# Performance work log

Hardware: AMD Instinct MI355X
Metric: run time of the kernel (lower is better)

The kernel has to match this reference:

```python
import jax, jax.numpy as jnp
import numpy as np
import math

H = 1024
N = 64          # d_state; complex modes = N // 2
N2 = N // 2
B = 8
L = 2048
DT_MIN, DT_MAX = 0.001, 0.1


def setup_inputs() -> dict:
    key = jax.random.key(0)
    ks = jax.random.split(key, 8)
    u = jax.random.normal(ks[0], (B, H, L), dtype=jnp.float32)
    # log_dt ~ Uniform[log(dt_min), log(dt_max)]
    log_dt = (jax.random.uniform(ks[1], (H,), dtype=jnp.float32)
              * (math.log(DT_MAX) - math.log(DT_MIN)) + math.log(DT_MIN))
    # random_dplr with scaling='inverse': real part 0.5, imag = (1/pi)*N*(N/(1+2n)-1)
    n = jnp.arange(N2, dtype=jnp.float32)
    w_real = 0.5 * jnp.ones((1, N2), dtype=jnp.float32)
    w_imag = ((1.0 / math.pi) * N * (N / (1.0 + 2.0 * n) - 1.0))[None, :].astype(jnp.float32)
    log_w_real = jnp.log(w_real + 1e-4)  # module stores log(-w.real + 1e-4)
    # C = randn complex (channels=1, H, N2), scaled by normalized B (folded into randn here)
    C_re = jax.random.normal(ks[2], (1, H, N2), dtype=jnp.float32) / math.sqrt(2 * N2)
    C_im = jax.random.normal(ks[3], (1, H, N2), dtype=jnp.float32) / math.sqrt(2 * N2)
    D = jax.random.normal(ks[4], (1, H), dtype=jnp.float32)
    # output_linear: Conv1d(k=1) from channels*H -> H  => weight (H, H)
    W_out = jax.random.normal(ks[5], (H, H), dtype=jnp.float32) / math.sqrt(H)
    b_out = jax.random.normal(ks[6], (H,), dtype=jnp.float32) * 0.01
    return {"u": u, "log_dt": log_dt, "log_w_real": log_w_real, "w_imag": w_imag,
            "C_re": C_re, "C_im": C_im, "D": D, "W_out": W_out, "b_out": b_out}


def reference(u, log_dt, log_w_real, w_imag, C_re, C_im, D, W_out, b_out):
    b, h, l = u.shape
    # --- SSKernelDiag.forward ---
    dt = jnp.exp(log_dt)                                   # (H,)
    w = -jnp.exp(log_w_real) + 1j * w_imag                 # (n_ssm=1, N2)
    w = jnp.broadcast_to(w, (h, w.shape[-1]))              # repeat copies -> (H, N2)
    dtA = w * dt[:, None]                                  # (H, N2) complex
    C = (C_re + 1j * C_im) * (jnp.exp(dtA) - 1.0) / w      # (c, H, N2)
    # Vandermonde: exp(dtA * arange(L)) -> (H, N2, L) complex
    K = jnp.exp(dtA[:, :, None] * jnp.arange(l, dtype=jnp.float32))
    k = 2.0 * jnp.einsum('chn,hnl->chl', C, K).real        # (c, H, L) float
    # --- FFT convolution ---
    k_f = jnp.fft.rfft(k, n=2 * l)                         # (c, H, L+1)
    u_f = jnp.fft.rfft(u, n=2 * l)                         # (B, H, L+1)
    y_f = jnp.einsum('bhl,chl->bchl', u_f, k_f)
    y = jnp.fft.irfft(y_f, n=2 * l)[..., :l]               # (B, c, H, L)
    # skip connection with D
    y = y + jnp.einsum('bhl,ch->bchl', u, D)
    y = y.reshape(b, -1, l)                                # (B, c*H, L)
    y = jax.nn.gelu(y, approximate=False)
    # output 1x1 conv: (B, c*H, L) x (H, c*H) -> (B, H, L)
    y = jnp.einsum('bil,oi->bol', y, W_out) + b_out[None, :, None]
    return y
```

## Files before the change

kernel.cpp:

```cpp
#include <hip/hip_runtime.h>
#include <hip/hip_bf16.h>

#define HH 1024
#define LL 2048
#define BB 8
#define NN2 32
#define CT 128
#define NCH 16

typedef short bf16x8 __attribute__((ext_vector_type(8)));
typedef float f32x4  __attribute__((ext_vector_type(4)));

static __device__ __forceinline__ unsigned short bfbits(float x) {
    __hip_bfloat16 h = __float2bfloat16(x);
    return *(unsigned short*)&h;
}
static __device__ __forceinline__ float f_from_bits(unsigned short b) {
    __hip_bfloat16 h; *(unsigned short*)&h = b; return __bfloat162float(h);
}
static __device__ __forceinline__ float2 cexp_n(float2 dA, float p) {
    float mag = __expf(dA.x * p);
    float rev = dA.y * p * 0.15915494309f;
    rev -= floorf(rev);
    float ang = rev * 6.28318530718f;
    return make_float2(mag * __cosf(ang), mag * __sinf(ang));
}

#define SWZ(off, row) ((off) ^ (((row) & 7) << 4))

__global__ __launch_bounds__(256) void aux_tables(
    const float* __restrict__ log_dt, const float* __restrict__ log_w_real,
    const float* __restrict__ w_imag, const float* __restrict__ C_re,
    const float* __restrict__ C_im,
    __hip_bfloat16* __restrict__ AJ_g, __hip_bfloat16* __restrict__ AP_g,
    float* __restrict__ misc_g)
{
    __shared__ float2 dtA_s[NN2];
    __shared__ float2 Cn_s[NN2];
    const int tid = threadIdx.x;
    const int h = blockIdx.x;

    if (tid < NN2) {
        int n = tid;
        float dt = expf(log_dt[h]);
        float wr = -expf(log_w_real[n]);
        float wi = w_imag[n];
        float dar = wr * dt, dai = wi * dt;
        dtA_s[n] = make_float2(dar, dai);
        float er = expf(dar);
        float sn, cs; sincosf(dai, &sn, &cs);
        float exr = er * cs - 1.0f, exi = er * sn;
        float den = wr * wr + wi * wi;
        float fr = (exr * wr + exi * wi) / den;
        float fi = (exi * wr - exr * wi) / den;
        float cre = C_re[h * NN2 + n], cim = C_im[h * NN2 + n];
        float2 Cv = make_float2(cre * fr - cim * fi, cre * fi + cim * fr);
        Cn_s[n] = Cv;
        misc_g[h * 256 + 128 + 2 * n]     = Cv.x;
        misc_g[h * 256 + 128 + 2 * n + 1] = Cv.y;
        float magA = expf(dar * 128.0f);
        float snA, csA; sincosf(dai * 128.0f, &snA, &csA);
        misc_g[h * 256 + 192 + 2 * n]     = magA * csA;
        misc_g[h * 256 + 192 + 2 * n + 1] = magA * snA;
    }
    __syncthreads();

    char* ajb = (char*)AJ_g + (size_t)h * 16384;
    #pragma unroll
    for (int q = 0; q < 2; ++q) {
        int task = q * 256 + tid;
        int n = task >> 4, j0 = (task & 15) * 8;
        float2 dA = dtA_s[n];
        unsigned rw[4], iw[4];
        #pragma unroll
        for (int i2 = 0; i2 < 4; ++i2) {
            float2 a0 = cexp_n(dA, (float)(127 - j0 - 2 * i2));
            float2 a1 = cexp_n(dA, (float)(127 - j0 - 2 * i2 - 1));
            rw[i2] = (unsigned)bfbits(a0.x) | ((unsigned)bfbits(a1.x) << 16);
            iw[i2] = (unsigned)bfbits(a0.y) | ((unsigned)bfbits(a1.y) << 16);
        }
        int r0 = 2 * n, r1 = 2 * n + 1;
        *(uint4*)(ajb + SWZ(r0 * 256 + j0 * 2, r0)) = make_uint4(rw[0], rw[1], rw[2], rw[3]);
        *(uint4*)(ajb + SWZ(r1 * 256 + j0 * 2, r1)) = make_uint4(iw[0], iw[1], iw[2], iw[3]);
    }

    char* apb = (char*)AP_g + (size_t)h * 16384;
    #pragma unroll
    for (int q = 0; q < 2; ++q) {
        int task = q * 256 + tid;
        int ttr = task >> 2, n0 = (task & 3) * 8;
        unsigned w[8];
        #pragma unroll
        for (int i = 0; i < 8; ++i) {
            float2 a = cexp_n(dtA_s[n0 + i], (float)(ttr + 1));
            w[i] = (unsigned)bfbits(2.0f * a.x) | ((unsigned)bfbits(-2.0f * a.y) << 16);
        }
        *(uint4*)(apb + SWZ(ttr * 128 + n0 * 4, ttr))      = make_uint4(w[0], w[1], w[2], w[3]);
        *(uint4*)(apb + SWZ(ttr * 128 + n0 * 4 + 16, ttr)) = make_uint4(w[4], w[5], w[6], w[7]);
    }

    {
        int t = tid >> 1, nb = (tid & 1) * 16;
        float s = 0.f;
        #pragma unroll
        for (int i = 0; i < 16; ++i) {
            int n = nb + i;
            float2 a = cexp_n(dtA_s[n], (float)t);
            float2 C = Cn_s[n];
            s += C.x * a.x - C.y * a.y;
        }
        s += __shfl_xor(s, 1);
        if ((tid & 1) == 0) misc_g[h * 256 + t] = 2.0f * s;
    }
}

#define S_U    0
#define S_UN   16384
#define S_P    32768
#define S_KT   40960
#define S_TOT  41984

#define KBUILD(hf)                                                       \
    _Pragma("unroll")                                                    \
    for (int q = 0; q < 4; ++q) {                                        \
        int idx = q * 512 + tid;                                         \
        int ttr = idx >> 4, j0 = (idx & 15) * 4;                         \
        int base = ttr - (hf) * 64 - j0;                                 \
        ushort4 o;                                                       \
        o.x = (base     >= 0) ? bfbits(kt[base])     : (unsigned short)0;\
        o.y = (base - 1 >= 0) ? bfbits(kt[base - 1]) : (unsigned short)0;\
        o.z = (base - 2 >= 0) ? bfbits(kt[base - 2]) : (unsigned short)0;\
        o.w = (base - 3 >= 0) ? bfbits(kt[base - 3]) : (unsigned short)0;\
        *(ushort4*)(smem + SWZ(S_UN + ttr * 128 + j0 * 2, ttr)) = o;     \
    }

__global__ __launch_bounds__(512, 6) void ssm_mfma(
    const float* __restrict__ u,
    const __hip_bfloat16* __restrict__ AJ_g,
    const __hip_bfloat16* __restrict__ AP_g,
    const float* __restrict__ misc_g,
    const float* __restrict__ Dp, __hip_bfloat16* __restrict__ g_out)
{
    extern __shared__ char smem[];
    float*  kt   = (float*)(smem + S_KT);
    float2* CnL  = (float2*)(smem + S_KT + 512);
    float2* A128 = (float2*)(smem + S_KT + 768);

    const int tid  = threadIdx.x;
    const int lane = tid & 63;
    const int wave = tid >> 6;
    const int wm   = wave >> 2;
    const int wn   = wave & 3;
    const int h    = blockIdx.x;
    const int bh   = blockIdx.y;

    {
        const char* ajs = (const char*)AJ_g + (size_t)h * 16384;
        __builtin_amdgcn_global_load_lds(
            (const __attribute__((address_space(1))) void*)(ajs + tid * 16),
            (__attribute__((address_space(3))) void*)(smem + S_UN + wave * 1024), 16, 0, 0);
        __builtin_amdgcn_global_load_lds(
            (const __attribute__((address_space(1))) void*)(ajs + 8192 + tid * 16),
            (__attribute__((address_space(3))) void*)(smem + S_UN + 8192 + wave * 1024), 16, 0, 0);
        if (tid < 64) {
            const char* ms = (const char*)misc_g + (size_t)h * 1024;
            __builtin_amdgcn_global_load_lds(
                (const __attribute__((address_space(1))) void*)(ms + tid * 16),
                (__attribute__((address_space(3))) void*)(smem + S_KT), 16, 0, 0);
        }
    }

    float4 ureg[4];
    #pragma unroll
    for (int q = 0; q < 4; ++q) {
        int b = bh * 4 + q;
        ureg[q] = *(const float4*)(u + ((size_t)(b * HH + h)) * LL + tid * 4);
    }
    #pragma unroll
    for (int q = 0; q < 4; ++q) {
        int row = q * 16 + (tid >> 5);
        int j   = (tid & 31) * 4;
        ushort4 o;
        o.x = bfbits(ureg[q].x); o.y = bfbits(ureg[q].y);
        o.z = bfbits(ureg[q].z); o.w = bfbits(ureg[q].w);
        *(ushort4*)(smem + SWZ(S_U + row * 256 + j * 2, row)) = o;
    }
    asm volatile("s_waitcnt vmcnt(0)" ::: "memory");
    __syncthreads();

    f32x4 accP[2] = {};
    #pragma unroll
    for (int ks = 0; ks < 4; ++ks) {
        int kf = ks * 32 + (lane >> 4) * 8;
        bf16x8 a0, a1, b0;
        {
            int r = wm * 32 + (lane & 15);
            a0 = *(bf16x8*)(smem + SWZ(S_U + r * 256 + kf * 2, r));
            int r2 = r + 16;
            a1 = *(bf16x8*)(smem + SWZ(S_U + r2 * 256 + kf * 2, r2));
        }
        {
            int r = wn * 16 + (lane & 15);
            b0 = *(bf16x8*)(smem + SWZ(S_UN + r * 256 + kf * 2, r));
        }
        accP[0] = __builtin_amdgcn_mfma_f32_16x16x32_bf16(a0, b0, accP[0], 0, 0, 0);
        accP[1] = __builtin_amdgcn_mfma_f32_16x16x32_bf16(a1, b0, accP[1], 0, 0, 0);
    }
    #pragma unroll
    for (int mt = 0; mt < 2; ++mt)
        #pragma unroll
        for (int r = 0; r < 4; ++r) {
            int row = wm * 32 + mt * 16 + (lane >> 4) * 4 + r;
            int col = wn * 16 + (lane & 15);
            *(unsigned short*)(smem + SWZ(S_P + row * 128 + col * 2, row)) =
                bfbits(accP[mt][r]);
        }
    __syncthreads();

    KBUILD(0)
    if (tid < 128) {
        int b = tid >> 5, n = tid & 31;
        float2 C = CnL[n];
        float2 A = A128[n];
        float sr = 0.f, si = 0.f;
        for (int c = 0; c < NCH; ++c) {
            int row = b * 16 + c;
            int off = SWZ(S_P + row * 128 + n * 4, row);
            unsigned int pv = *(unsigned int*)(smem + off);
            float pr = f_from_bits((unsigned short)(pv & 0xffff));
            float pi = f_from_bits((unsigned short)(pv >> 16));
            float csr = C.x * sr - C.y * si;
            float csi = C.x * si + C.y * sr;
            *(unsigned int*)(smem + off) =
                (unsigned)bfbits(csr) | ((unsigned)bfbits(csi) << 16);
            float nsr = A.x * sr - A.y * si + pr;
            float nsi = A.x * si + A.y * sr + pi;
            sr = nsr; si = nsi;
        }
    }
    __syncthreads();

    f32x4 acc[2][2] = {};
    #pragma unroll
    for (int ks = 0; ks < 2; ++ks) {
        int kf = ks * 32 + (lane >> 4) * 8;
        bf16x8 a0, a1, bv[2];
        {
            int r = wm * 32 + (lane & 15);
            a0 = *(bf16x8*)(smem + SWZ(S_U + r * 256 + kf * 2, r));
            int r2 = r + 16;
            a1 = *(bf16x8*)(smem + SWZ(S_U + r2 * 256 + kf * 2, r2));
        }
        #pragma unroll
        for (int nt = 0; nt < 2; ++nt) {
            int ttr = wn * 32 + nt * 16 + (lane & 15);
            bv[nt] = *(bf16x8*)(smem + SWZ(S_UN + ttr * 128 + kf * 2, ttr));
        }
        #pragma unroll
        for (int nt = 0; nt < 2; ++nt) {
            acc[0][nt] = __builtin_amdgcn_mfma_f32_16x16x32_bf16(a0, bv[nt], acc[0][nt], 0, 0, 0);
            acc[1][nt] = __builtin_amdgcn_mfma_f32_16x16x32_bf16(a1, bv[nt], acc[1][nt], 0, 0, 0);
        }
    }
    __syncthreads();

    KBUILD(1)
    __syncthreads();
    #pragma unroll
    for (int ks = 0; ks < 2; ++ks) {
        int kf = ks * 32 + (lane >> 4) * 8;
        bf16x8 a0, a1, bv[2];
        {
            int r = wm * 32 + (lane & 15);
            a0 = *(bf16x8*)(smem + SWZ(S_U + r * 256 + 128 + kf * 2, r));
            int r2 = r + 16;
            a1 = *(bf16x8*)(smem + SWZ(S_U + r2 * 256 + 128 + kf * 2, r2));
        }
        #pragma unroll
        for (int nt = 0; nt < 2; ++nt) {
            int ttr = wn * 32 + nt * 16 + (lane & 15);
            bv[nt] = *(bf16x8*)(smem + SWZ(S_UN + ttr * 128 + kf * 2, ttr));
        }
        #pragma unroll
        for (int nt = 0; nt < 2; ++nt) {
            acc[0][nt] = __builtin_amdgcn_mfma_f32_16x16x32_bf16(a0, bv[nt], acc[0][nt], 0, 0, 0);
            acc[1][nt] = __builtin_amdgcn_mfma_f32_16x16x32_bf16(a1, bv[nt], acc[1][nt], 0, 0, 0);
        }
    }
    __syncthreads();

    {
        const char* aps = (const char*)AP_g + (size_t)h * 16384;
        __builtin_amdgcn_global_load_lds(
            (const __attribute__((address_space(1))) void*)(aps + tid * 16),
            (__attribute__((address_space(3))) void*)(smem + S_UN + wave * 1024), 16, 0, 0);
        __builtin_amdgcn_global_load_lds(
            (const __attribute__((address_space(1))) void*)(aps + 8192 + tid * 16),
            (__attribute__((address_space(3))) void*)(smem + S_UN + 8192 + wave * 1024), 16, 0, 0);
    }
    asm volatile("s_waitcnt vmcnt(0)" ::: "memory");
    __syncthreads();

    #pragma unroll
    for (int ks = 0; ks < 2; ++ks) {
        int kf = ks * 32 + (lane >> 4) * 8;
        bf16x8 a0, a1, bv[2];
        {
            int r = wm * 32 + (lane & 15);
            a0 = *(bf16x8*)(smem + SWZ(S_P + r * 128 + kf * 2, r));
            int r2 = r + 16;
            a1 = *(bf16x8*)(smem + SWZ(S_P + r2 * 128 + kf * 2, r2));
        }
        #pragma unroll
        for (int nt = 0; nt < 2; ++nt) {
            int ttr = wn * 32 + nt * 16 + (lane & 15);
            bv[nt] = *(bf16x8*)(smem + SWZ(S_UN + ttr * 128 + kf * 2, ttr));
        }
        #pragma unroll
        for (int nt = 0; nt < 2; ++nt) {
            acc[0][nt] = __builtin_amdgcn_mfma_f32_16x16x32_bf16(a0, bv[nt], acc[0][nt], 0, 0, 0);
            acc[1][nt] = __builtin_amdgcn_mfma_f32_16x16x32_bf16(a1, bv[nt], acc[1][nt], 0, 0, 0);
        }
    }

    const float Dv = Dp[h];
    #pragma unroll
    for (int mt = 0; mt < 2; ++mt)
        #pragma unroll
        for (int nt = 0; nt < 2; ++nt)
            #pragma unroll
            for (int r = 0; r < 4; ++r) {
                int row = wm * 32 + mt * 16 + (lane >> 4) * 4 + r;
                int ttr = wn * 32 + nt * 16 + (lane & 15);
                int off = SWZ(S_U + row * 256 + ttr * 2, row);
                float uv = f_from_bits(*(unsigned short*)(smem + off));
                float y = acc[mt][nt][r] + Dv * uv;
                float z = 0.7978845608f * (y + 0.044715f * y * y * y);
                float e = __expf(2.0f * z);
                float th = 1.0f - 2.0f / (e + 1.0f);
                float gel = 0.5f * y * (1.0f + th);
                *(unsigned short*)(smem + off) = bfbits(gel);
            }
    __syncthreads();
    #pragma unroll
    for (int q = 0; q < 2; ++q) {
        int flat = q * 512 + tid;
        int row = flat >> 4, c16 = flat & 15;
        uint4 v = *(uint4*)(smem + SWZ(S_U + row * 256 + c16 * 16, row));
        int b = bh * 4 + (row >> 4), c = row & 15;
        *(uint4*)(g_out + ((size_t)(b * HH + h)) * LL + c * CT + c16 * 8) = v;
    }
}

__global__ __launch_bounds__(256) void conv_w(
    const float* __restrict__ W, __hip_bfloat16* __restrict__ Wb)
{
    int i = blockIdx.x * 256 + threadIdx.x;
    float4 v = ((const float4*)W)[i];
    ushort4 o;
    o.x = bfbits(v.x); o.y = bfbits(v.y); o.z = bfbits(v.z); o.w = bfbits(v.w);
    ((ushort4*)Wb)[i] = o;
}

__global__ __launch_bounds__(256) void transpose_g(
    const __hip_bfloat16* __restrict__ g, __hip_bfloat16* __restrict__ gT)
{
    __shared__ __hip_bfloat16 t[64][66];
    const int tid = threadIdx.x;
    const int b  = blockIdx.z;
    const int h0 = blockIdx.x * 64;
    const int l0 = blockIdx.y * 64;

    #pragma unroll
    for (int q = 0; q < 2; ++q) {
        int idx = tid + q * 256;
        int r = idx >> 3, c8 = (idx & 7) * 8;
        uint4 v = *(const uint4*)(g + ((size_t)(b * HH + h0 + r)) * LL + l0 + c8);
        unsigned int* dst = (unsigned int*)&t[r][c8];
        dst[0] = v.x; dst[1] = v.y; dst[2] = v.z; dst[3] = v.w;
    }
    __syncthreads();
    #pragma unroll
    for (int q = 0; q < 2; ++q) {
        int idx = tid + q * 256;
        int r = idx >> 3, c8 = (idx & 7) * 8;
        unsigned short tmp[8];
        #pragma unroll
        for (int j = 0; j < 8; ++j) tmp[j] = *(unsigned short*)&t[c8 + j][r];
        uint4 o;
        o.x = (unsigned)tmp[0] | ((unsigned)tmp[1] << 16);
        o.y = (unsigned)tmp[2] | ((unsigned)tmp[3] << 16);
        o.z = (unsigned)tmp[4] | ((unsigned)tmp[5] << 16);
        o.w = (unsigned)tmp[6] | ((unsigned)tmp[7] << 16);
        *(uint4*)(gT + ((size_t)(b * LL + l0 + r)) * HH + h0 + c8) = o;
    }
}

#define GSLOT 32768
#define STAGE_TILE(kt_, s_)                                                      \
    {                                                                            \
        const int k0_ = (kt_) * 64;                                              \
        _Pragma("unroll")                                                        \
        for (int v_ = 0; v_ < 4; ++v_) {                                         \
            int row_ = v_ * 64 + rsub;                                           \
            const __hip_bfloat16* ga_ = Wb + (size_t)(o0 + row_) * HH + k0_ + csw; \
            const __hip_bfloat16* gb_ = gT + (size_t)(n0 + row_) * HH + k0_ + csw; \
            char* dA_ = smem + (s_) * GSLOT + (v_ * 64 + wave * 8) * 128;        \
            char* dB_ = smem + 2 * GSLOT + (s_) * GSLOT + (v_ * 64 + wave * 8) * 128; \
            __builtin_amdgcn_global_load_lds(                                    \
                (const __attribute__((address_space(1))) void*)ga_,              \
                (__attribute__((address_space(3))) void*)dA_, 16, 0, 0);         \
            __builtin_amdgcn_global_load_lds(                                    \
                (const __attribute__((address_space(1))) void*)gb_,              \
                (__attribute__((address_space(3))) void*)dB_, 16, 0, 0);         \
        }                                                                        \
    }

#define COMPUTE_TILE(s_)                                                         \
    {                                                                            \
        const char* baseA = smem + (s_) * GSLOT;                                 \
        const char* baseB = smem + 2 * GSLOT + (s_) * GSLOT;                     \
        bf16x8 bfr[4][2];                                                        \
        _Pragma("unroll")                                                        \
        for (int nt = 0; nt < 4; ++nt)                                           \
            _Pragma("unroll")                                                    \
            for (int ks = 0; ks < 2; ++ks) {                                     \
                int rb = wn * 64 + nt * 16 + (lane & 15);                        \
                int c  = (ks * 32 + (lane >> 4) * 8) ^ ((rb & 7) << 3);          \
                bfr[nt][ks] = *(const bf16x8*)(baseB + rb * 128 + c * 2);        \
            }                                                                    \
        _Pragma("unroll")                                                        \
        for (int qq = 0; qq < 4; ++qq) {                                         \
            bf16x8 af[2][2];                                                     \
            _Pragma("unroll")                                                    \
            for (int mt = 0; mt < 2; ++mt)                                       \
                _Pragma("unroll")                                                \
                for (int ks = 0; ks < 2; ++ks) {                                 \
                    int ra = wm * 128 + (qq * 2 + mt) * 16 + (lane & 15);        \
                    int c  = (ks * 32 + (lane >> 4) * 8) ^ ((ra & 7) << 3);      \
                    af[mt][ks] = *(const bf16x8*)(baseA + ra * 128 + c * 2);     \
                }                                                                \
            __builtin_amdgcn_s_setprio(1);                                       \
            _Pragma("unroll")                                                    \
            for (int mt = 0; mt < 2; ++mt)                                       \
                _Pragma("unroll")                                                \
                for (int nt = 0; nt < 4; ++nt) {                                 \
                    acc[qq * 2 + mt][nt] = __builtin_amdgcn_mfma_f32_16x16x32_bf16( \
                        af[mt][0], bfr[nt][0], acc[qq * 2 + mt][nt], 0, 0, 0);   \
                    acc[qq * 2 + mt][nt] = __builtin_amdgcn_mfma_f32_16x16x32_bf16( \
                        af[mt][1], bfr[nt][1], acc[qq * 2 + mt][nt], 0, 0, 0);   \
                }                                                                \
            __builtin_amdgcn_s_setprio(0);                                       \
        }                                                                        \
    }

__global__ __launch_bounds__(512, 2) void out_gemm_256(
    const __hip_bfloat16* __restrict__ Wb,
    const __hip_bfloat16* __restrict__ gT,
    const float* __restrict__ bias,
    float* __restrict__ out)
{
    extern __shared__ char smem[];
    const int tid  = threadIdx.x;
    const int lane = tid & 63;
    const int wave = tid >> 6;
    const int wm = wave >> 2;
    const int wn = wave & 3;

    int wg  = blockIdx.x;
    int swz = (wg & 7) * 32 + (wg >> 3);
    const int o0 = (swz & 3) * 256;
    const int n0 = (swz >> 2) * 256;

    const int rsub = tid >> 3;
    const int csw  = ((tid & 7) ^ (rsub & 7)) << 3;

    f32x4 acc[8][4] = {};

    STAGE_TILE(0, 0)
    STAGE_TILE(1, 1)

    for (int t = 0; t < 15; ++t) {
        asm volatile("s_waitcnt vmcnt(8)" ::: "memory");
        __builtin_amdgcn_s_barrier();
        __builtin_amdgcn_sched_barrier(0);
        COMPUTE_TILE(t & 1)
        asm volatile("s_waitcnt lgkmcnt(0)" ::: "memory");
        __builtin_amdgcn_s_barrier();
        __builtin_amdgcn_sched_barrier(0);
        if (t < 14) STAGE_TILE(t + 2, t & 1)
    }
    asm volatile("s_waitcnt vmcnt(0)" ::: "memory");
    __builtin_amdgcn_s_barrier();
    __builtin_amdgcn_sched_barrier(0);
    COMPUTE_TILE(1)

    const int bb = n0 >> 11;
    #pragma unroll
    for (int m = 0; m < 8; ++m) {
        int o = o0 + wm * 128 + m * 16 + (lane >> 4) * 4;
        #pragma unroll
        for (int nt = 0; nt < 4; ++nt) {
            int n = n0 + wn * 64 + nt * 16 + (lane & 15);
            int l = n & 2047;
            #pragma unroll
            for (int r = 0; r < 4; ++r)
                out[((size_t)(bb * HH + o + r)) * LL + l] = acc[m][nt][r] + bias[o + r];
        }
    }
}

extern "C" void kernel_launch(void* const* d_in, const int* in_sizes, int n_in,
                              void* d_out, int out_size, void* d_ws, size_t ws_size,
                              hipStream_t stream) {
    const float* u          = (const float*)d_in[0];
    const float* log_dt     = (const float*)d_in[1];
    const float* log_w_real = (const float*)d_in[2];
    const float* w_imag     = (const float*)d_in[3];
    const float* C_re       = (const float*)d_in[4];
    const float* C_im       = (const float*)d_in[5];
    const float* Dp         = (const float*)d_in[6];
    const float* W          = (const float*)d_in[7];
    const float* bias       = (const float*)d_in[8];
    float* out = (float*)d_out;

    __hip_bfloat16* AJ_g = (__hip_bfloat16*)d_out;
    __hip_bfloat16* AP_g = (__hip_bfloat16*)((char*)d_out + 16777216);
    __hip_bfloat16* g    = (__hip_bfloat16*)((char*)d_out + 33554432);
    __hip_bfloat16* gT     = (__hip_bfloat16*)d_ws;
    __hip_bfloat16* Wb     = (__hip_bfloat16*)((char*)d_ws + 33554432);
    float*          misc_g = (float*)((char*)d_ws + 35651584);

    hipFuncSetAttribute((const void*)ssm_mfma,
                        hipFuncAttributeMaxDynamicSharedMemorySize, S_TOT);
    hipFuncSetAttribute((const void*)out_gemm_256,
                        hipFuncAttributeMaxDynamicSharedMemorySize, 131072);

    conv_w<<<dim3(HH * HH / 1024), 256, 0, stream>>>(W, Wb);
    aux_tables<<<dim3(HH), 256, 0, stream>>>(log_dt, log_w_real, w_imag,
                                             C_re, C_im, AJ_g, AP_g, misc_g);
    ssm_mfma<<<dim3(HH, 2), 512, S_TOT, stream>>>(u, AJ_g, AP_g, misc_g, Dp, g);
    transpose_g<<<dim3(HH / 64, LL / 64, BB), 256, 0, stream>>>(g, gT);
    out_gemm_256<<<dim3(256), 512, 131072, stream>>>(Wb, gT, bias, out);
}
```

Baseline: 108.4 us.

## Process all eight batches per block in SSM kernel to reuse per-channel tables

The SSM chunked-scan kernel now handles all 8 batch rows for a channel in one block instead of splitting batches across two blocks. Each wave computes a larger 32x64 output tile, so the per-channel AJ/AP tables and kernel Toeplitz builds are loaded and built once per channel rather than twice. In exchange, shared memory per block grows and occupancy hints drop from 6 to 4 blocks, and the grid halves to 1024 blocks, which lowers parallelism.

```diff
diff --git a/kernel.cpp b/kernel.cpp
--- a/kernel.cpp
+++ b/kernel.cpp
@@ -115,10 +115,10 @@
 }
 
 #define S_U    0
-#define S_UN   16384
-#define S_P    32768
-#define S_KT   40960
-#define S_TOT  41984
+#define S_UN   32768
+#define S_P    49152
+#define S_KT   65536
+#define S_TOT  66560
 
 #define KBUILD(hf)                                                       \
     _Pragma("unroll")                                                    \
@@ -134,7 +134,7 @@
         *(ushort4*)(smem + SWZ(S_UN + ttr * 128 + j0 * 2, ttr)) = o;     \
     }
 
-__global__ __launch_bounds__(512, 6) void ssm_mfma(
+__global__ __launch_bounds__(512, 4) void ssm_mfma(
     const float* __restrict__ u,
     const __hip_bfloat16* __restrict__ AJ_g,
     const __hip_bfloat16* __restrict__ AP_g,
@@ -149,10 +149,9 @@
     const int tid  = threadIdx.x;
     const int lane = tid & 63;
     const int wave = tid >> 6;
-    const int wm   = wave >> 2;
-    const int wn   = wave & 3;
+    const int wr4  = wave >> 1;
+    const int wc2  = wave & 1;
     const int h    = blockIdx.x;
-    const int bh   = blockIdx.y;
 
     {
         const char* ajs = (const char*)AJ_g + (size_t)h * 16384;
@@ -170,14 +169,12 @@
         }
     }
 
-    float4 ureg[4];
-    #pragma unroll
-    for (int q = 0; q < 4; ++q) {
-        int b = bh * 4 + q;
-        ureg[q] = *(const float4*)(u + ((size_t)(b * HH + h)) * LL + tid * 4);
-    }
-    #pragma unroll
-    for (int q = 0; q < 4; ++q) {
+    float4 ureg[8];
+    #pragma unroll
+    for (int q = 0; q < 8; ++q)
+        ureg[q] = *(const float4*)(u + ((size_t)(q * HH + h)) * LL + tid * 4);
+    #pragma unroll
+    for (int q = 0; q < 8; ++q) {
         int row = q * 16 + (tid >> 5);
         int j   = (tid & 31) * 4;
         ushort4 o;
@@ -188,37 +185,43 @@
     asm volatile("s_waitcnt vmcnt(0)" ::: "memory");
     __syncthreads();
 
-    f32x4 accP[2] = {};
+    f32x4 accP[2][2] = {};
     #pragma unroll
     for (int ks = 0; ks < 4; ++ks) {
         int kf = ks * 32 + (lane >> 4) * 8;
-        bf16x8 a0, a1, b0;
+        bf16x8 a0, a1, b0, b1;
         {
-            int r = wm * 32 + (lane & 15);
+            int r = wr4 * 32 + (lane & 15);
             a0 = *(bf16x8*)(smem + SWZ(S_U + r * 256 + kf * 2, r));
             int r2 = r + 16;
             a1 = *(bf16x8*)(smem + SWZ(S_U + r2 * 256 + kf * 2, r2));
         }
         {
-            int r = wn * 16 + (lane & 15);
+            int r = wc2 * 32 + (lane & 15);
             b0 = *(bf16x8*)(smem + SWZ(S_UN + r * 256 + kf * 2, r));
-        }
-        accP[0] = __builtin_amdgcn_mfma_f32_16x16x32_bf16(a0, b0, accP[0], 0, 0, 0);
-        accP[1] = __builtin_amdgcn_mfma_f32_16x16x32_bf16(a1, b0, accP[1], 0, 0, 0);
+            int r2 = r + 16;
+            b1 = *(bf16x8*)(smem + SWZ(S_UN + r2 * 256 + kf * 2, r2));
+        }
+        accP[0][0] = __builtin_amdgcn_mfma_f32_16x16x32_bf16(a0, b0, accP[0][0], 0, 0, 0);
+        accP[0][1] = __builtin_amdgcn_mfma_f32_16x16x32_bf16(a0, b1, accP[0][1], 0, 0, 0);
+        accP[1][0] = __builtin_amdgcn_mfma_f32_16x16x32_bf16(a1, b0, accP[1][0], 0, 0, 0);
+        accP[1][1] = __builtin_amdgcn_mfma_f32_16x16x32_bf16(a1, b1, accP[1][1], 0, 0, 0);
     }
     #pragma unroll
     for (int mt = 0; mt < 2; ++mt)
         #pragma unroll
-        for (int r = 0; r < 4; ++r) {
-            int row = wm * 32 + mt * 16 + (lane >> 4) * 4 + r;
-            int col = wn * 16 + (lane & 15);
-            *(unsigned short*)(smem + SWZ(S_P + row * 128 + col * 2, row)) =
-                bfbits(accP[mt][r]);
-        }
+        for (int nt = 0; nt < 2; ++nt)
+            #pragma unroll
+            for (int r = 0; r < 4; ++r) {
+                int row = wr4 * 32 + mt * 16 + (lane >> 4) * 4 + r;
+                int col = wc2 * 32 + nt * 16 + (lane & 15);
+                *(unsigned short*)(smem + SWZ(S_P + row * 128 + col * 2, row)) =
+                    bfbits(accP[mt][nt][r]);
+            }
     __syncthreads();
 
     KBUILD(0)
-    if (tid < 128) {
+    if (tid < 256) {
         int b = tid >> 5, n = tid & 31;
         float2 C = CnL[n];
         float2 A = A128[n];
@@ -240,24 +243,24 @@
     }
     __syncthreads();
 
-    f32x4 acc[2][2] = {};
+    f32x4 acc[2][4] = {};
     #pragma unroll
     for (int ks = 0; ks < 2; ++ks) {
         int kf = ks * 32 + (lane >> 4) * 8;
-        bf16x8 a0, a1, bv[2];
+        bf16x8 a0, a1, bv[4];
         {
-            int r = wm * 32 + (lane & 15);
+            int r = wr4 * 32 + (lane & 15);
             a0 = *(bf16x8*)(smem + SWZ(S_U + r * 256 + kf * 2, r));
             int r2 = r + 16;
             a1 = *(bf16x8*)(smem + SWZ(S_U + r2 * 256 + kf * 2, r2));
         }
         #pragma unroll
-        for (int nt = 0; nt < 2; ++nt) {
-            int ttr = wn * 32 + nt * 16 + (lane & 15);
+        for (int nt = 0; nt < 4; ++nt) {
+            int ttr = wc2 * 64 + nt * 16 + (lane & 15);
             bv[nt] = *(bf16x8*)(smem + SWZ(S_UN + ttr * 128 + kf * 2, ttr));
         }
         #pragma unroll
-        for (int nt = 0; nt < 2; ++nt) {
+        for (int nt = 0; nt < 4; ++nt) {
             acc[0][nt] = __builtin_amdgcn_mfma_f32_16x16x32_bf16(a0, bv[nt], acc[0][nt], 0, 0, 0);
             acc[1][nt] = __builtin_amdgcn_mfma_f32_16x16x32_bf16(a1, bv[nt], acc[1][nt], 0, 0, 0);
         }
@@ -269,20 +272,20 @@
     #pragma unroll
     for (int ks = 0; ks < 2; ++ks) {
         int kf = ks * 32 + (lane >> 4) * 8;
-        bf16x8 a0, a1, bv[2];
+        bf16x8 a0, a1, bv[4];
         {
-            int r = wm * 32 + (lane & 15);
+            int r = wr4 * 32 + (lane & 15);
             a0 = *(bf16x8*)(smem + SWZ(S_U + r * 256 + 128 + kf * 2, r));
             int r2 = r + 16;
             a1 = *(bf16x8*)(smem + SWZ(S_U + r2 * 256 + 128 + kf * 2, r2));
         }
         #pragma unroll
-        for (int nt = 0; nt < 2; ++nt) {
-            int ttr = wn * 32 + nt * 16 + (lane & 15);
+        for (int nt = 0; nt < 4; ++nt) {
+            int ttr = wc2 * 64 + nt * 16 + (lane & 15);
             bv[nt] = *(bf16x8*)(smem + SWZ(S_UN + ttr * 128 + kf * 2, ttr));
         }
         #pragma unroll
-        for (int nt = 0; nt < 2; ++nt) {
+        for (int nt = 0; nt < 4; ++nt) {
             acc[0][nt] = __builtin_amdgcn_mfma_f32_16x16x32_bf16(a0, bv[nt], acc[0][nt], 0, 0, 0);
             acc[1][nt] = __builtin_amdgcn_mfma_f32_16x16x32_bf16(a1, bv[nt], acc[1][nt], 0, 0, 0);
         }
@@ -304,20 +307,20 @@
     #pragma unroll
     for (int ks = 0; ks < 2; ++ks) {
         int kf = ks * 32 + (lane >> 4) * 8;
-        bf16x8 a0, a1, bv[2];
+        bf16x8 a0, a1, bv[4];
         {
-            int r = wm * 32 + (lane & 15);
+            int r = wr4 * 32 + (lane & 15);
             a0 = *(bf16x8*)(smem + SWZ(S_P + r * 128 + kf * 2, r));
             int r2 = r + 16;
             a1 = *(bf16x8*)(smem + SWZ(S_P + r2 * 128 + kf * 2, r2));
         }
         #pragma unroll
-        for (int nt = 0; nt < 2; ++nt) {
-            int ttr = wn * 32 + nt * 16 + (lane & 15);
+        for (int nt = 0; nt < 4; ++nt) {
+            int ttr = wc2 * 64 + nt * 16 + (lane & 15);
             bv[nt] = *(bf16x8*)(smem + SWZ(S_UN + ttr * 128 + kf * 2, ttr));
         }
         #pragma unroll
-        for (int nt = 0; nt < 2; ++nt) {
+        for (int nt = 0; nt < 4; ++nt) {
             acc[0][nt] = __builtin_amdgcn_mfma_f32_16x16x32_bf16(a0, bv[nt], acc[0][nt], 0, 0, 0);
             acc[1][nt] = __builtin_amdgcn_mfma_f32_16x16x32_bf16(a1, bv[nt], acc[1][nt], 0, 0, 0);
         }
@@ -327,11 +330,11 @@
     #pragma unroll
     for (int mt = 0; mt < 2; ++mt)
         #pragma unroll
-        for (int nt = 0; nt < 2; ++nt)
+        for (int nt = 0; nt < 4; ++nt)
             #pragma unroll
             for (int r = 0; r < 4; ++r) {
-                int row = wm * 32 + mt * 16 + (lane >> 4) * 4 + r;
-                int ttr = wn * 32 + nt * 16 + (lane & 15);
+                int row = wr4 * 32 + mt * 16 + (lane >> 4) * 4 + r;
+                int ttr = wc2 * 64 + nt * 16 + (lane & 15);
                 int off = SWZ(S_U + row * 256 + ttr * 2, row);
                 float uv = f_from_bits(*(unsigned short*)(smem + off));
                 float y = acc[mt][nt][r] + Dv * uv;
@@ -343,11 +346,11 @@
             }
     __syncthreads();
     #pragma unroll
-    for (int q = 0; q < 2; ++q) {
+    for (int q = 0; q < 4; ++q) {
         int flat = q * 512 + tid;
         int row = flat >> 4, c16 = flat & 15;
         uint4 v = *(uint4*)(smem + SWZ(S_U + row * 256 + c16 * 16, row));
-        int b = bh * 4 + (row >> 4), c = row & 15;
+        int b = row >> 4, c = row & 15;
         *(uint4*)(g_out + ((size_t)(b * HH + h)) * LL + c * CT + c16 * 8) = v;
     }
 }
@@ -539,7 +542,7 @@
     conv_w<<<dim3(HH * HH / 1024), 256, 0, stream>>>(W, Wb);
     aux_tables<<<dim3(HH), 256, 0, stream>>>(log_dt, log_w_real, w_imag,
                                              C_re, C_im, AJ_g, AP_g, misc_g);
-    ssm_mfma<<<dim3(HH, 2), 512, S_TOT, stream>>>(u, AJ_g, AP_g, misc_g, Dp, g);
+    ssm_mfma<<<dim3(HH), 512, S_TOT, stream>>>(u, AJ_g, AP_g, misc_g, Dp, g);
     transpose_g<<<dim3(HH / 64, LL / 64, BB), 256, 0, stream>>>(g, gT);
     out_gemm_256<<<dim3(256), 512, 131072, stream>>>(Wb, gT, bias, out);
 }
```

Measured after the change: 107.6 us. Within noise of the previous version (-0.8%).

## Fold weight conversion into aux kernel and merge intra-chunk Toeplitz GEMM passes

Applied to the files above, without the earlier changes.

The standalone W-to-bf16 conversion kernel is folded into aux_tables, which removes one launch. In ssm_mfma, the two half-K Toeplitz GEMM passes, each with its own KBUILD and barriers, become one K=128 pass. That pass reads from eight shifted copies of the reversed kernel, built once before the state GEMM. The state recurrence now preloads its P values into registers and runs before the Toeplitz MMA with no barrier between them, cutting several syncthreads and the LDS rebuild work at the cost of extra LDS (S_TOT grows).

```diff
diff --git a/kernel.cpp b/kernel.cpp
--- a/kernel.cpp
+++ b/kernel.cpp
@@ -31,14 +31,21 @@
 __global__ __launch_bounds__(256) void aux_tables(
     const float* __restrict__ log_dt, const float* __restrict__ log_w_real,
     const float* __restrict__ w_imag, const float* __restrict__ C_re,
-    const float* __restrict__ C_im,
+    const float* __restrict__ C_im, const float* __restrict__ W,
     __hip_bfloat16* __restrict__ AJ_g, __hip_bfloat16* __restrict__ AP_g,
-    float* __restrict__ misc_g)
+    float* __restrict__ misc_g, __hip_bfloat16* __restrict__ Wb)
 {
     __shared__ float2 dtA_s[NN2];
     __shared__ float2 Cn_s[NN2];
     const int tid = threadIdx.x;
     const int h = blockIdx.x;
+
+    {
+        float4 v = ((const float4*)(W + (size_t)h * HH))[tid];
+        ushort4 o;
+        o.x = bfbits(v.x); o.y = bfbits(v.y); o.z = bfbits(v.z); o.w = bfbits(v.w);
+        ((ushort4*)(Wb + (size_t)h * HH))[tid] = o;
+    }
 
     if (tid < NN2) {
         int n = tid;
@@ -118,21 +125,8 @@
 #define S_UN   16384
 #define S_P    32768
 #define S_KT   40960
-#define S_TOT  41984
-
-#define KBUILD(hf)                                                       \
-    _Pragma("unroll")                                                    \
-    for (int q = 0; q < 4; ++q) {                                        \
-        int idx = q * 512 + tid;                                         \
-        int ttr = idx >> 4, j0 = (idx & 15) * 4;                         \
-        int base = ttr - (hf) * 64 - j0;                                 \
-        ushort4 o;                                                       \
-        o.x = (base     >= 0) ? bfbits(kt[base])     : (unsigned short)0;\
-        o.y = (base - 1 >= 0) ? bfbits(kt[base - 1]) : (unsigned short)0;\
-        o.z = (base - 2 >= 0) ? bfbits(kt[base - 2]) : (unsigned short)0;\
-        o.w = (base - 3 >= 0) ? bfbits(kt[base - 3]) : (unsigned short)0;\
-        *(ushort4*)(smem + SWZ(S_UN + ttr * 128 + j0 * 2, ttr)) = o;     \
-    }
+#define S_KTP  41984
+#define S_TOT  46208
 
 __global__ __launch_bounds__(512, 6) void ssm_mfma(
     const float* __restrict__ u,
@@ -188,6 +182,21 @@
     asm volatile("s_waitcnt vmcnt(0)" ::: "memory");
     __syncthreads();
 
+    {
+        int s = wave;
+        int i0 = lane * 4;
+        ushort4 o;
+        #pragma unroll
+        for (int k = 0; k < 4; ++k) {
+            int src = 127 - s - (i0 + k);
+            ((unsigned short*)&o)[k] = (src >= 0) ? bfbits(kt[src]) : (unsigned short)0;
+        }
+        *(ushort4*)(smem + S_KTP + s * 528 + i0 * 2) = o;
+        if (lane < 2) {
+            *(ushort4*)(smem + S_KTP + s * 528 + 512 + lane * 8) = make_ushort4(0, 0, 0, 0);
+        }
+    }
+
     f32x4 accP[2] = {};
     #pragma unroll
     for (int ks = 0; ks < 4; ++ks) {
@@ -217,78 +226,6 @@
         }
     __syncthreads();
 
-    KBUILD(0)
-    if (tid < 128) {
-        int b = tid >> 5, n = tid & 31;
-        float2 C = CnL[n];
-        float2 A = A128[n];
-        float sr = 0.f, si = 0.f;
-        for (int c = 0; c < NCH; ++c) {
-            int row = b * 16 + c;
-            int off = SWZ(S_P + row * 128 + n * 4, row);
-            unsigned int pv = *(unsigned int*)(smem + off);
-            float pr = f_from_bits((unsigned short)(pv & 0xffff));
-            float pi = f_from_bits((unsigned short)(pv >> 16));
-            float csr = C.x * sr - C.y * si;
-            float csi = C.x * si + C.y * sr;
-            *(unsigned int*)(smem + off) =
-                (unsigned)bfbits(csr) | ((unsigned)bfbits(csi) << 16);
-            float nsr = A.x * sr - A.y * si + pr;
-            float nsi = A.x * si + A.y * sr + pi;
-            sr = nsr; si = nsi;
-        }
-    }
-    __syncthreads();
-
-    f32x4 acc[2][2] = {};
-    #pragma unroll
-    for (int ks = 0; ks < 2; ++ks) {
-        int kf = ks * 32 + (lane >> 4) * 8;
-        bf16x8 a0, a1, bv[2];
-        {
-            int r = wm * 32 + (lane & 15);
-            a0 = *(bf16x8*)(smem + SWZ(S_U + r * 256 + kf * 2, r));
-            int r2 = r + 16;
-            a1 = *(bf16x8*)(smem + SWZ(S_U + r2 * 256 + kf * 2, r2));
-        }
-        #pragma unroll
-        for (int nt = 0; nt < 2; ++nt) {
-            int ttr = wn * 32 + nt * 16 + (lane & 15);
-            bv[nt] = *(bf16x8*)(smem + SWZ(S_UN + ttr * 128 + kf * 2, ttr));
-        }
-        #pragma unroll
-        for (int nt = 0; nt < 2; ++nt) {
-            acc[0][nt] = __builtin_amdgcn_mfma_f32_16x16x32_bf16(a0, bv[nt], acc[0][nt], 0, 0, 0);
-            acc[1][nt] = __builtin_amdgcn_mfma_f32_16x16x32_bf16(a1, bv[nt], acc[1][nt], 0, 0, 0);
-        }
-    }
-    __syncthreads();
-
-    KBUILD(1)
-    __syncthreads();
-    #pragma unroll
-    for (int ks = 0; ks < 2; ++ks) {
-        int kf = ks * 32 + (lane >> 4) * 8;
-        bf16x8 a0, a1, bv[2];
-        {
-            int r = wm * 32 + (lane & 15);
-            a0 = *(bf16x8*)(smem + SWZ(S_U + r * 256 + 128 + kf * 2, r));
-            int r2 = r + 16;
-            a1 = *(bf16x8*)(smem + SWZ(S_U + r2 * 256 + 128 + kf * 2, r2));
-        }
-        #pragma unroll
-        for (int nt = 0; nt < 2; ++nt) {
-            int ttr = wn * 32 + nt * 16 + (lane & 15);
-            bv[nt] = *(bf16x8*)(smem + SWZ(S_UN + ttr * 128 + kf * 2, ttr));
-        }
-        #pragma unroll
-        for (int nt = 0; nt < 2; ++nt) {
-            acc[0][nt] = __builtin_amdgcn_mfma_f32_16x16x32_bf16(a0, bv[nt], acc[0][nt], 0, 0, 0);
-            acc[1][nt] = __builtin_amdgcn_mfma_f32_16x16x32_bf16(a1, bv[nt], acc[1][nt], 0, 0, 0);
-        }
-    }
-    __syncthreads();
-
     {
         const char* aps = (const char*)AP_g + (size_t)h * 16384;
         __builtin_amdgcn_global_load_lds(
@@ -297,6 +234,58 @@
         __builtin_amdgcn_global_load_lds(
             (const __attribute__((address_space(1))) void*)(aps + 8192 + tid * 16),
             (__attribute__((address_space(3))) void*)(smem + S_UN + 8192 + wave * 1024), 16, 0, 0);
+    }
+
+    if (tid < 128) {
+        int b = tid >> 5, n = tid & 31;
+        float2 C = CnL[n];
+        float2 A = A128[n];
+        unsigned int pv[NCH];
+        int offs[NCH];
+        #pragma unroll
+        for (int c = 0; c < NCH; ++c) {
+            int row = b * 16 + c;
+            offs[c] = SWZ(S_P + row * 128 + n * 4, row);
+            pv[c] = *(unsigned int*)(smem + offs[c]);
+        }
+        float sr = 0.f, si = 0.f;
+        #pragma unroll
+        for (int c = 0; c < NCH; ++c) {
+            float pr = f_from_bits((unsigned short)(pv[c] & 0xffff));
+            float pi = f_from_bits((unsigned short)(pv[c] >> 16));
+            float csr = C.x * sr - C.y * si;
+            float csi = C.x * si + C.y * sr;
+            *(unsigned int*)(smem + offs[c]) =
+                (unsigned)bfbits(csr) | ((unsigned)bfbits(csi) << 16);
+            float nsr = A.x * sr - A.y * si + pr;
+            float nsi = A.x * si + A.y * sr + pi;
+            sr = nsr; si = nsi;
+        }
+    }
+
+    f32x4 acc[2][2] = {};
+    #pragma unroll
+    for (int ks = 0; ks < 4; ++ks) {
+        int kf = ks * 32 + (lane >> 4) * 8;
+        bf16x8 a0, a1, bv[2];
+        {
+            int r = wm * 32 + (lane & 15);
+            a0 = *(bf16x8*)(smem + SWZ(S_U + r * 256 + kf * 2, r));
+            int r2 = r + 16;
+            a1 = *(bf16x8*)(smem + SWZ(S_U + r2 * 256 + kf * 2, r2));
+        }
+        #pragma unroll
+        for (int nt = 0; nt < 2; ++nt) {
+            int ttr = wn * 32 + nt * 16 + (lane & 15);
+            int s   = (127 - ttr) & 7;
+            int gq  = (127 - ttr + kf) >> 3;
+            bv[nt] = *(bf16x8*)(smem + S_KTP + s * 528 + gq * 16);
+        }
+        #pragma unroll
+        for (int nt = 0; nt < 2; ++nt) {
+            acc[0][nt] = __builtin_amdgcn_mfma_f32_16x16x32_bf16(a0, bv[nt], acc[0][nt], 0, 0, 0);
+            acc[1][nt] = __builtin_amdgcn_mfma_f32_16x16x32_bf16(a1, bv[nt], acc[1][nt], 0, 0, 0);
+        }
     }
     asm volatile("s_waitcnt vmcnt(0)" ::: "memory");
     __syncthreads();
@@ -350,16 +339,6 @@
         int b = bh * 4 + (row >> 4), c = row & 15;
         *(uint4*)(g_out + ((size_t)(b * HH + h)) * LL + c * CT + c16 * 8) = v;
     }
-}
-
-__global__ __launch_bounds__(256) void conv_w(
-    const float* __restrict__ W, __hip_bfloat16* __restrict__ Wb)
-{
-    int i = blockIdx.x * 256 + threadIdx.x;
-    float4 v = ((const float4*)W)[i];
-    ushort4 o;
-    o.x = bfbits(v.x); o.y = bfbits(v.y); o.z = bfbits(v.z); o.w = bfbits(v.w);
-    ((ushort4*)Wb)[i] = o;
 }
 
 __global__ __launch_bounds__(256) void transpose_g(
@@ -536,9 +515,8 @@
     hipFuncSetAttribute((const void*)out_gemm_256,
                         hipFuncAttributeMaxDynamicSharedMemorySize, 131072);
 
-    conv_w<<<dim3(HH * HH / 1024), 256, 0, stream>>>(W, Wb);
     aux_tables<<<dim3(HH), 256, 0, stream>>>(log_dt, log_w_real, w_imag,
-                                             C_re, C_im, AJ_g, AP_g, misc_g);
+                                             C_re, C_im, W, AJ_g, AP_g, misc_g, Wb);
     ssm_mfma<<<dim3(HH, 2), 512, S_TOT, stream>>>(u, AJ_g, AP_g, misc_g, Dp, g);
     transpose_g<<<dim3(HH / 64, LL / 64, BB), 256, 0, stream>>>(g, gT);
     out_gemm_256<<<dim3(256), 512, 131072, stream>>>(Wb, gT, bias, out);
```

After: 101.0 us. 6.8% less time.
